# Performance work log

Measured on AMD Instinct MI355X. Metric: run time of the kernel, lower is better.

## Reference

```python
import jax, jax.numpy as jnp
import numpy as np

NDIM = 3
RADIUS = 0.14
MAX_GRID_DIM = 96
MAX_COLLISIONS = 128
B, N, M, C = 4, 4096, 4096, 16


def setup_inputs() -> dict:
    key = jax.random.key(0)
    k1, k2, k3 = jax.random.split(key, 3)
    locs = jax.random.uniform(k1, (B, N, NDIM), dtype=jnp.float32)
    data = jax.random.normal(k2, (B, N, C), dtype=jnp.float32)
    qlocs = jax.random.uniform(k3, (B, M, NDIM), dtype=jnp.float32)
    return {"locs": locs, "data": data, "qlocs": qlocs}


def _hashgrid_idxs(locs, radius, max_grid_dim):
    """Replicates hashgrid_order: assign each particle a flat grid-cell ID and
    return the permutation (new -> old index) that sorts particles by cell."""
    lower = locs.min(axis=1)                                   # [B,D]
    upper = locs.max(axis=1)                                   # [B,D]
    grid_dims = jnp.ceil(jnp.clip((upper - lower) / radius, 0.0, max_grid_dim))
    center = (lower + upper) * 0.5
    lower = center - grid_dims * radius * 0.5                  # grid lower corner
    cell = jnp.floor((locs - lower[:, None, :]) / radius)
    cell = jnp.clip(cell, 0.0, grid_dims[:, None, :] - 1.0).astype(jnp.int32)
    gd = jnp.maximum(grid_dims.astype(jnp.int32), 1)           # [B,D]
    # row-major strides per batch: stride[d] = prod(gd[d+1:])
    rev = jnp.cumprod(gd[:, ::-1], axis=1)[:, ::-1]            # [B,D]
    strides = jnp.concatenate(
        [rev[:, 1:], jnp.ones((gd.shape[0], 1), jnp.int32)], axis=1)
    cell_ids = (cell * strides[:, None, :]).sum(-1)            # [B,N]
    # stable sort by cell id -> idxs[b, i] = original index of particle now at i
    idxs = jnp.argsort(cell_ids, axis=1)
    return idxs


def reference(locs, data, qlocs):
    idxs = _hashgrid_idxs(locs, RADIUS, MAX_GRID_DIM)
    locs_r = jnp.take_along_axis(locs, idxs[..., None], axis=1)   # [B,N,D]
    data_r = jnp.take_along_axis(data, idxs[..., None], axis=1)   # [B,N,C]

    # Radius search of qlocs against the cell-sorted particles. Neighbor indices
    # are w.r.t. the reordered locs, listed in ascending reordered-index order
    # (cell order), capped at MAX_COLLISIONS, padded with -1.
    qn = (qlocs * qlocs).sum(-1)                                  # [B,M]
    pn = (locs_r * locs_r).sum(-1)                                # [B,N]
    cross = jnp.einsum('bmd,bnd->bmn', qlocs, locs_r)             # [B,M,N]
    dist2 = qn[:, :, None] + pn[:, None, :] - 2.0 * cross         # [B,M,N]
    mask = dist2 <= RADIUS * RADIUS
    # stable argsort of ~mask puts in-radius particles first, in index order
    order = jnp.argsort(~mask, axis=-1)
    neighbors = order[..., :MAX_COLLISIONS].astype(jnp.int32)     # [B,M,K]
    count = mask.sum(-1)                                          # [B,M]
    valid = jnp.arange(MAX_COLLISIONS) < count[..., None]
    neighbors = jnp.where(valid, neighbors, jnp.int32(-1))
    return locs_r, data_r, idxs.astype(jnp.int32), neighbors
```

## Files before the change

### kernel.cpp

```cpp
#include <hip/hip_runtime.h>
#include <stdint.h>

#define BB 4
#define NN 4096
#define MM 4096
#define CC 16
#define KMAX 128

static constexpr int LOCSR_OFF = 0;
static constexpr int DATAR_OFF = BB * NN * 3;
static constexpr int IDXS_OFF  = DATAR_OFF + BB * NN * CC;
static constexpr int NB_OFF    = IDXS_OFF + BB * NN;

static constexpr float RAD_F = 0.14f;
static constexpr float R2F   = (float)(0.14 * 0.14);

__global__ void __launch_bounds__(256) k_bbox(const float* __restrict__ locs,
                                              float* __restrict__ pmm) {
    int blk = blockIdx.x;
    int b = blk >> 4, s = blk & 15, t = threadIdx.x;
    int i = s * 256 + t;
    const float* p = locs + (b * NN + i) * 3;
    float x0 = p[0], x1 = p[1], x2 = p[2];
    __shared__ float sm[6][256];
    sm[0][t] = x0; sm[1][t] = x1; sm[2][t] = x2;
    sm[3][t] = x0; sm[4][t] = x1; sm[5][t] = x2;
    __syncthreads();
    for (int st = 128; st > 0; st >>= 1) {
        if (t < st) {
            sm[0][t] = fminf(sm[0][t], sm[0][t + st]);
            sm[1][t] = fminf(sm[1][t], sm[1][t + st]);
            sm[2][t] = fminf(sm[2][t], sm[2][t + st]);
            sm[3][t] = fmaxf(sm[3][t], sm[3][t + st]);
            sm[4][t] = fmaxf(sm[4][t], sm[4][t + st]);
            sm[5][t] = fmaxf(sm[5][t], sm[5][t + st]);
        }
        __syncthreads();
    }
    if (t == 0) {
        float* o = pmm + blk * 6;
        o[0] = sm[0][0]; o[1] = sm[1][0]; o[2] = sm[2][0];
        o[3] = sm[3][0]; o[4] = sm[4][0]; o[5] = sm[5][0];
    }
}

__global__ void __launch_bounds__(1024) k_rank(const float* __restrict__ locs,
                                               const float* __restrict__ data,
                                               const float* __restrict__ pmm,
                                               float* __restrict__ out,
                                               float4* __restrict__ sp4,
                                               unsigned* __restrict__ cs_sorted,
                                               float* __restrict__ gp) {
    __shared__ uint4 keys4[NN / 4];
    __shared__ int partial[16][64];
    __shared__ int s_dst[64];
    __shared__ float sp_low[3], sp_gdf[3];
    __shared__ int sp_s0, sp_s1;
    int blk = blockIdx.x;
    int b = blk >> 6;
    int t = threadIdx.x;
    int wave = t >> 6, lane = t & 63;

    if (t == 0) {
        const float* pm = pmm + b * 96;
        float mn0 = 1e30f, mn1 = 1e30f, mn2 = 1e30f;
        float mx0 = -1e30f, mx1 = -1e30f, mx2 = -1e30f;
#pragma unroll
        for (int k = 0; k < 16; ++k) {
            mn0 = fminf(mn0, pm[k * 6 + 0]);
            mn1 = fminf(mn1, pm[k * 6 + 1]);
            mn2 = fminf(mn2, pm[k * 6 + 2]);
            mx0 = fmaxf(mx0, pm[k * 6 + 3]);
            mx1 = fmaxf(mx1, pm[k * 6 + 4]);
            mx2 = fmaxf(mx2, pm[k * 6 + 5]);
        }
        float lo[3] = {mn0, mn1, mn2}, up[3] = {mx0, mx1, mx2};
        float low2[3], gdf[3];
        int gdi[3];
#pragma unroll
        for (int d = 0; d < 3; ++d) {
            float u = __fdiv_rn(__fsub_rn(up[d], lo[d]), RAD_F);
            u = fminf(fmaxf(u, 0.0f), 96.0f);
            float g = ceilf(u);
            float center = __fmul_rn(__fadd_rn(lo[d], up[d]), 0.5f);
            low2[d] = __fsub_rn(center, __fmul_rn(__fmul_rn(g, RAD_F), 0.5f));
            gdf[d] = g;
            gdi[d] = max((int)g, 1);
        }
        sp_low[0] = low2[0]; sp_low[1] = low2[1]; sp_low[2] = low2[2];
        sp_gdf[0] = gdf[0];  sp_gdf[1] = gdf[1];  sp_gdf[2] = gdf[2];
        sp_s0 = gdi[1] * gdi[2];
        sp_s1 = gdi[2];
        if ((blk & 63) == 0) {
            float* o = gp + b * 12;
            o[0] = low2[0]; o[1] = low2[1]; o[2] = low2[2];
            o[3] = gdf[0];  o[4] = gdf[1];  o[5] = gdf[2];
            ((int*)o)[6]  = gdi[1] * gdi[2];
            ((int*)o)[7]  = gdi[2];
            ((int*)o)[8]  = gdi[0] * gdi[1] * gdi[2];
            ((int*)o)[9]  = gdi[0];
            ((int*)o)[10] = gdi[1];
            ((int*)o)[11] = gdi[2];
        }
    }
    __syncthreads();

    {
        float l0 = sp_low[0], l1 = sp_low[1], l2 = sp_low[2];
        float g0 = sp_gdf[0], g1 = sp_gdf[1], g2 = sp_gdf[2];
        int s0 = sp_s0, s1 = sp_s1;
        const float4* lp = (const float4*)(locs + b * NN * 3) + t * 3;
        float4 A = lp[0], Bv = lp[1], Cv = lp[2];
        float ex[4] = {A.x, A.w, Bv.z, Cv.y};
        float ey[4] = {A.y, Bv.x, Bv.w, Cv.z};
        float ez[4] = {A.z, Bv.y, Cv.x, Cv.w};
        unsigned kk[4];
#pragma unroll
        for (int j = 0; j < 4; ++j) {
            float c0 = fminf(fmaxf(floorf(__fdiv_rn(__fsub_rn(ex[j], l0), RAD_F)), 0.0f), __fsub_rn(g0, 1.0f));
            float c1 = fminf(fmaxf(floorf(__fdiv_rn(__fsub_rn(ey[j], l1), RAD_F)), 0.0f), __fsub_rn(g1, 1.0f));
            float c2 = fminf(fmaxf(floorf(__fdiv_rn(__fsub_rn(ez[j], l2), RAD_F)), 0.0f), __fsub_rn(g2, 1.0f));
            unsigned cell = (unsigned)((int)c0 * s0 + (int)c1 * s1 + (int)c2);
            kk[j] = cell * 4096u + (unsigned)(4 * t + j);
        }
        keys4[t] = make_uint4(kk[0], kk[1], kk[2], kk[3]);
    }
    __syncthreads();

    int i = (blk & 63) * 64 + lane;
    unsigned key = ((const unsigned*)keys4)[i];
    uint4 mv = keys4[wave * 64 + lane];
    int rank = 0;
#pragma unroll
    for (int s = 0; s < 64; ++s) {
        unsigned a  = (unsigned)__builtin_amdgcn_readlane((int)mv.x, s);
        unsigned b2 = (unsigned)__builtin_amdgcn_readlane((int)mv.y, s);
        unsigned c2 = (unsigned)__builtin_amdgcn_readlane((int)mv.z, s);
        unsigned d2 = (unsigned)__builtin_amdgcn_readlane((int)mv.w, s);
        rank += (int)(a < key) + (int)(b2 < key) + (int)(c2 < key) + (int)(d2 < key);
    }
    partial[wave][lane] = rank;
    __syncthreads();
    if (wave == 0) {
        int r = 0;
#pragma unroll
        for (int w = 0; w < 16; ++w) r += partial[w][lane];
        s_dst[lane] = r;
    }
    __syncthreads();
    if (wave == 0) {
        int src = b * NN + i;
        int dst = b * NN + s_dst[lane];
        float x = locs[src * 3 + 0], y = locs[src * 3 + 1], z = locs[src * 3 + 2];
        out[IDXS_OFF + dst] = (float)i;
        out[LOCSR_OFF + dst * 3 + 0] = x;
        out[LOCSR_OFF + dst * 3 + 1] = y;
        out[LOCSR_OFF + dst * 3 + 2] = z;
        cs_sorted[dst] = key;
        float pn = __fadd_rn(__fadd_rn(__fmul_rn(x, x), __fmul_rn(y, y)), __fmul_rn(z, z));
        sp4[dst] = make_float4(x, y, z, pn);
    } else if (wave <= 4) {
        int p = lane;
        int ii = (blk & 63) * 64 + p;
        int dst = b * NN + s_dst[p];
        int c = wave - 1;
        const float4* dsrc = (const float4*)(data + (b * NN + ii) * 16);
        float4* ddst = (float4*)(out + DATAR_OFF + dst * 16);
        ddst[c] = dsrc[c];
    }
}

__device__ inline void axis_range(float qd, float lo, int gd, int* c0, int* c1) {
    const float DL = RAD_F + 1e-4f;
    float vlo = (qd - DL - lo) / RAD_F;
    float vhi = (qd + DL - lo) / RAD_F;
    int a = (int)floorf(vlo), b = (int)floorf(vhi);
    *c0 = min(max(a, 0), gd - 1);
    *c1 = min(max(b, 0), gd - 1);
}

__global__ void __launch_bounds__(256, 6) k_neighbors(const float* __restrict__ qlocs,
                                                      const float4* __restrict__ sp4,
                                                      const unsigned* __restrict__ cs_sorted,
                                                      const float* __restrict__ gp,
                                                      float* __restrict__ out) {
    __shared__ uint4 skeys4[NN / 4];
    const unsigned* skeys = (const unsigned*)skeys4;

    int blk = blockIdx.x;
    int b = blk >> 10;
    int t = threadIdx.x;
    int wave = t >> 6, lane = t & 63;

    {
        const uint4* g = (const uint4*)(cs_sorted + b * NN);
#pragma unroll
        for (int j = 0; j < 4; ++j) skeys4[t + 256 * j] = g[t + 256 * j];
    }

    int m = (blk & 1023) * 4 + wave;
    const float* o = gp + b * 12;
    const int* oi = (const int*)o;
    int s0 = oi[6], s1 = oi[7];
    int gd0 = oi[9], gd1 = oi[10], gd2 = oi[11];
    const float* q = qlocs + (b * MM + m) * 3;
    float q0 = q[0], q1 = q[1], q2 = q[2];
    float qn = __fadd_rn(__fadd_rn(__fmul_rn(q0, q0), __fmul_rn(q1, q1)), __fmul_rn(q2, q2));
    int cx0, cx1, cy0, cy1, cz0, cz1;
    axis_range(q0, o[0], gd0, &cx0, &cx1);
    axis_range(q1, o[1], gd1, &cy0, &cy1);
    axis_range(q2, o[2], gd2, &cz0, &cz1);
    const float4* sp = sp4 + b * NN;
    float* nb = out + NB_OFF + (b * MM + m) * KMAX;

    unsigned t0_[9], t1_[9];
    bool va_[9];
#pragma unroll
    for (int dx = 0; dx < 3; ++dx) {
#pragma unroll
        for (int dy = 0; dy < 3; ++dy) {
            int k = dx * 3 + dy;
            int cx = cx0 + dx, cy = cy0 + dy;
            bool v = (cx <= cx1) && (cy <= cy1);
            int base = cx * s0 + cy * s1;
            va_[k] = v;
            t0_[k] = v ? (unsigned)(base + cz0) * 4096u : 0u;
            t1_[k] = v ? (unsigned)(base + cz1 + 1) * 4096u : 0u;
        }
    }
    __syncthreads();

    unsigned tgt = 0u;
#pragma unroll
    for (int k = 0; k < 9; ++k) {
        tgt = (lane == k)      ? t0_[k] : tgt;
        tgt = (lane == 16 + k) ? t1_[k] : tgt;
    }
    int lo = 0, hi = NN;
#pragma unroll
    for (int it = 0; it < 12; ++it) {
        int mid = (lo + hi) >> 1;
        unsigned v = skeys[mid];
        bool c = v < tgt;
        lo = c ? mid + 1 : lo;
        hi = c ? hi : mid;
    }
    int res = lo;

    int ps_[9], pe_[9];
#pragma unroll
    for (int k = 0; k < 9; ++k) {
        int a = __shfl(res, k);
        int e = __shfl(res, 16 + k);
        ps_[k] = va_[k] ? a : 0;
        pe_[k] = va_[k] ? e : 0;
    }
    int pre_[10];
    pre_[0] = 0;
#pragma unroll
    for (int k = 0; k < 9; ++k) pre_[k + 1] = pre_[k] + max(pe_[k] - ps_[k], 0);
    int T = pre_[9];

    int count = 0;
    for (int l0i = 0; l0i < T; l0i += 64) {
        int l = l0i + lane;
        int p = 0;
#pragma unroll
        for (int k = 0; k < 9; ++k) {
            bool in = (l >= pre_[k]) && (l < pre_[k + 1]);
            p = in ? (ps_[k] + (l - pre_[k])) : p;
        }
        float4 P = sp[p];
        float cross = fmaf(q2, P.z, fmaf(q1, P.y, __fmul_rn(q0, P.x)));
        float dist2 = __fsub_rn(__fadd_rn(qn, P.w), __fmul_rn(2.0f, cross));
        bool hit = (l < T) && (dist2 <= R2F);
        unsigned long long bal = __ballot(hit);
        if (hit) {
            int pos = count + __popcll(bal & ((1ull << lane) - 1ull));
            if (pos < KMAX) nb[pos] = (float)p;
        }
        count += __popcll(bal);
        if (count >= KMAX) break;
    }
    for (int j = count + lane; j < KMAX; j += 64) nb[j] = -1.0f;
}

extern "C" void kernel_launch(void* const* d_in, const int* in_sizes, int n_in,
                              void* d_out, int out_size, void* d_ws, size_t ws_size,
                              hipStream_t stream) {
    const float* locs  = (const float*)d_in[0];
    const float* data  = (const float*)d_in[1];
    const float* qlocs = (const float*)d_in[2];
    float* out = (float*)d_out;
    char* ws = (char*)d_ws;
    float*    gp        = (float*)ws;
    float*    pmm       = (float*)(ws + 512);
    unsigned* cs_sorted = (unsigned*)(ws + 4608);
    float4*   sp4       = (float4*)(ws + 4608 + 65536);

    k_bbox<<<BB * 16, 256, 0, stream>>>(locs, pmm);
    k_rank<<<BB * 64, 1024, 0, stream>>>(locs, data, pmm, out, sp4, cs_sorted, gp);
    k_neighbors<<<BB * 1024, 256, 0, stream>>>(qlocs, sp4, cs_sorted, gp, out);
}
```

Before: 91.48 us.

## Fuse bounding-box reduction into rank kernel and double neighbor block size

Removes the separate k_bbox launch. Each k_rank block now computes the per-batch min/max itself, using wave shuffles followed by a small shared-memory reduction over the locs it already loads. This saves one kernel launch and a global round trip, but every one of the 64 blocks per batch repeats the full bbox reduction. Separately, k_neighbors now uses 512-thread blocks handling 8 queries each, so each 16KB shared key load is amortised over twice as many queries, at the cost of fewer and larger blocks.

New measurement: 89.96 us. No clear change (-1.7%).

```diff
diff --git a/kernel.cpp b/kernel.cpp
--- a/kernel.cpp
+++ b/kernel.cpp
@@ -15,38 +15,8 @@
 static constexpr float RAD_F = 0.14f;
 static constexpr float R2F   = (float)(0.14 * 0.14);
 
-__global__ void __launch_bounds__(256) k_bbox(const float* __restrict__ locs,
-                                              float* __restrict__ pmm) {
-    int blk = blockIdx.x;
-    int b = blk >> 4, s = blk & 15, t = threadIdx.x;
-    int i = s * 256 + t;
-    const float* p = locs + (b * NN + i) * 3;
-    float x0 = p[0], x1 = p[1], x2 = p[2];
-    __shared__ float sm[6][256];
-    sm[0][t] = x0; sm[1][t] = x1; sm[2][t] = x2;
-    sm[3][t] = x0; sm[4][t] = x1; sm[5][t] = x2;
-    __syncthreads();
-    for (int st = 128; st > 0; st >>= 1) {
-        if (t < st) {
-            sm[0][t] = fminf(sm[0][t], sm[0][t + st]);
-            sm[1][t] = fminf(sm[1][t], sm[1][t + st]);
-            sm[2][t] = fminf(sm[2][t], sm[2][t + st]);
-            sm[3][t] = fmaxf(sm[3][t], sm[3][t + st]);
-            sm[4][t] = fmaxf(sm[4][t], sm[4][t + st]);
-            sm[5][t] = fmaxf(sm[5][t], sm[5][t + st]);
-        }
-        __syncthreads();
-    }
-    if (t == 0) {
-        float* o = pmm + blk * 6;
-        o[0] = sm[0][0]; o[1] = sm[1][0]; o[2] = sm[2][0];
-        o[3] = sm[3][0]; o[4] = sm[4][0]; o[5] = sm[5][0];
-    }
-}
-
 __global__ void __launch_bounds__(1024) k_rank(const float* __restrict__ locs,
                                                const float* __restrict__ data,
-                                               const float* __restrict__ pmm,
                                                float* __restrict__ out,
                                                float4* __restrict__ sp4,
                                                unsigned* __restrict__ cs_sorted,
@@ -54,6 +24,7 @@
     __shared__ uint4 keys4[NN / 4];
     __shared__ int partial[16][64];
     __shared__ int s_dst[64];
+    __shared__ float wred[16][6];
     __shared__ float sp_low[3], sp_gdf[3];
     __shared__ int sp_s0, sp_s1;
     int blk = blockIdx.x;
@@ -61,20 +32,46 @@
     int t = threadIdx.x;
     int wave = t >> 6, lane = t & 63;
 
+    const float4* lp = (const float4*)(locs + b * NN * 3) + t * 3;
+    float4 A = lp[0], Bv = lp[1], Cv = lp[2];
+    float ex[4] = {A.x, A.w, Bv.z, Cv.y};
+    float ey[4] = {A.y, Bv.x, Bv.w, Cv.z};
+    float ez[4] = {A.z, Bv.y, Cv.x, Cv.w};
+
+    float mn0 = fminf(fminf(ex[0], ex[1]), fminf(ex[2], ex[3]));
+    float mx0 = fmaxf(fmaxf(ex[0], ex[1]), fmaxf(ex[2], ex[3]));
+    float mn1 = fminf(fminf(ey[0], ey[1]), fminf(ey[2], ey[3]));
+    float mx1 = fmaxf(fmaxf(ey[0], ey[1]), fmaxf(ey[2], ey[3]));
+    float mn2 = fminf(fminf(ez[0], ez[1]), fminf(ez[2], ez[3]));
+    float mx2 = fmaxf(fmaxf(ez[0], ez[1]), fmaxf(ez[2], ez[3]));
+#pragma unroll
+    for (int off = 32; off > 0; off >>= 1) {
+        mn0 = fminf(mn0, __shfl_xor(mn0, off));
+        mx0 = fmaxf(mx0, __shfl_xor(mx0, off));
+        mn1 = fminf(mn1, __shfl_xor(mn1, off));
+        mx1 = fmaxf(mx1, __shfl_xor(mx1, off));
+        mn2 = fminf(mn2, __shfl_xor(mn2, off));
+        mx2 = fmaxf(mx2, __shfl_xor(mx2, off));
+    }
+    if (lane == 0) {
+        wred[wave][0] = mn0; wred[wave][1] = mn1; wred[wave][2] = mn2;
+        wred[wave][3] = mx0; wred[wave][4] = mx1; wred[wave][5] = mx2;
+    }
+    __syncthreads();
+
     if (t == 0) {
-        const float* pm = pmm + b * 96;
-        float mn0 = 1e30f, mn1 = 1e30f, mn2 = 1e30f;
-        float mx0 = -1e30f, mx1 = -1e30f, mx2 = -1e30f;
+        float a0 = 1e30f, a1 = 1e30f, a2 = 1e30f;
+        float u0 = -1e30f, u1 = -1e30f, u2 = -1e30f;
 #pragma unroll
         for (int k = 0; k < 16; ++k) {
-            mn0 = fminf(mn0, pm[k * 6 + 0]);
-            mn1 = fminf(mn1, pm[k * 6 + 1]);
-            mn2 = fminf(mn2, pm[k * 6 + 2]);
-            mx0 = fmaxf(mx0, pm[k * 6 + 3]);
-            mx1 = fmaxf(mx1, pm[k * 6 + 4]);
-            mx2 = fmaxf(mx2, pm[k * 6 + 5]);
-        }
-        float lo[3] = {mn0, mn1, mn2}, up[3] = {mx0, mx1, mx2};
+            a0 = fminf(a0, wred[k][0]);
+            a1 = fminf(a1, wred[k][1]);
+            a2 = fminf(a2, wred[k][2]);
+            u0 = fmaxf(u0, wred[k][3]);
+            u1 = fmaxf(u1, wred[k][4]);
+            u2 = fmaxf(u2, wred[k][5]);
+        }
+        float lo[3] = {a0, a1, a2}, up[3] = {u0, u1, u2};
         float low2[3], gdf[3];
         int gdi[3];
 #pragma unroll
@@ -109,11 +106,6 @@
         float l0 = sp_low[0], l1 = sp_low[1], l2 = sp_low[2];
         float g0 = sp_gdf[0], g1 = sp_gdf[1], g2 = sp_gdf[2];
         int s0 = sp_s0, s1 = sp_s1;
-        const float4* lp = (const float4*)(locs + b * NN * 3) + t * 3;
-        float4 A = lp[0], Bv = lp[1], Cv = lp[2];
-        float ex[4] = {A.x, A.w, Bv.z, Cv.y};
-        float ey[4] = {A.y, Bv.x, Bv.w, Cv.z};
-        float ez[4] = {A.z, Bv.y, Cv.x, Cv.w};
         unsigned kk[4];
 #pragma unroll
         for (int j = 0; j < 4; ++j) {
@@ -179,7 +171,7 @@
     *c1 = min(max(b, 0), gd - 1);
 }
 
-__global__ void __launch_bounds__(256, 6) k_neighbors(const float* __restrict__ qlocs,
+__global__ void __launch_bounds__(512, 6) k_neighbors(const float* __restrict__ qlocs,
                                                       const float4* __restrict__ sp4,
                                                       const unsigned* __restrict__ cs_sorted,
                                                       const float* __restrict__ gp,
@@ -188,17 +180,17 @@
     const unsigned* skeys = (const unsigned*)skeys4;
 
     int blk = blockIdx.x;
-    int b = blk >> 10;
+    int b = blk >> 9;
     int t = threadIdx.x;
     int wave = t >> 6, lane = t & 63;
 
     {
         const uint4* g = (const uint4*)(cs_sorted + b * NN);
 #pragma unroll
-        for (int j = 0; j < 4; ++j) skeys4[t + 256 * j] = g[t + 256 * j];
-    }
-
-    int m = (blk & 1023) * 4 + wave;
+        for (int j = 0; j < 8; ++j) skeys4[t + 512 * j] = g[t + 512 * j];
+    }
+
+    int m = (blk & 511) * 8 + wave;
     const float* o = gp + b * 12;
     const int* oi = (const int*)o;
     int s0 = oi[6], s1 = oi[7];
@@ -294,11 +286,9 @@
     float* out = (float*)d_out;
     char* ws = (char*)d_ws;
     float*    gp        = (float*)ws;
-    float*    pmm       = (float*)(ws + 512);
-    unsigned* cs_sorted = (unsigned*)(ws + 4608);
-    float4*   sp4       = (float4*)(ws + 4608 + 65536);
-
-    k_bbox<<<BB * 16, 256, 0, stream>>>(locs, pmm);
-    k_rank<<<BB * 64, 1024, 0, stream>>>(locs, data, pmm, out, sp4, cs_sorted, gp);
-    k_neighbors<<<BB * 1024, 256, 0, stream>>>(qlocs, sp4, cs_sorted, gp, out);
-}
+    unsigned* cs_sorted = (unsigned*)(ws + 512);
+    float4*   sp4       = (float4*)(ws + 512 + 65536);
+
+    k_rank<<<BB * 64, 1024, 0, stream>>>(locs, data, out, sp4, cs_sorted, gp);
+    k_neighbors<<<BB * 512, 512, 0, stream>>>(qlocs, sp4, cs_sorted, gp, out);
+}
```
